# Kernel optimization log

Hardware: AMD Instinct MI355X
Metric: run time of the kernel (lower is better)

The kernel has to match this reference:

```python
import jax, jax.numpy as jnp
import numpy as np

BM = 64; BN = 64          # block_m, block_n
NKM = BM // 4; NKN = BN // 4   # tokens sampled per block (16)
# topk_newtype bands: cumulative-pooled-attention fraction -> granularity value (0 = skip block)
RATIO_BANDS = [(1, 0.05), (2, 0.15), (4, 0.25), (8, 0.5)]


def setup_inputs() -> dict:
    key = jax.random.key(0)
    kq, kk, kv, ki, kj = jax.random.split(key, 5)
    B, H, L, D = 1, 8, 4096, 64
    q = jax.random.normal(kq, (B, H, L, D), jnp.float32)
    k = jax.random.normal(kk, (B, H, L, D), jnp.float32)
    v = jax.random.normal(kv, (B, H, L, D), jnp.float32)
    # distinct in-block sample positions, shared across blocks per (B,H)
    # (mirrors torch.topk(torch.rand(B,H,1,block), sample_num))
    sample_idx_q = jnp.argsort(jax.random.uniform(ki, (B, H, BM)), axis=-1)[..., :NKM].astype(jnp.int32)
    sample_idx_k = jnp.argsort(jax.random.uniform(kj, (B, H, BN)), axis=-1)[..., :NKN].astype(jnp.int32)
    return {"q": q, "k": k, "v": v, "sample_idx_q": sample_idx_q, "sample_idx_k": sample_idx_k}


def _sample_blocks(x, idx, bs, nk):
    # x: [B,H,L,D]; idx: [B,H,nk] in-block positions -> [B,H,nb*nk,D]
    B, H, L, D = x.shape
    nb = L // bs
    xb = x.reshape(B, H, nb, bs, D)
    gidx = jnp.broadcast_to(idx[:, :, None, :, None], (B, H, nb, nk, D))
    return jnp.take_along_axis(xb, gidx, axis=3).reshape(B, H, nb * nk, D)


def _block_mask(q, k, sample_idx_q, sample_idx_k):
    # pooled downsampled attention -> per-(q_block,k_block) keep mask (topk_newtype)
    B, H, L, D = q.shape
    qb, kb = L // BM, L // BN
    sq = _sample_blocks(q, sample_idx_q, BM, NKM)  # [B,H,qb*NKM,D]
    sk = _sample_blocks(k, sample_idx_k, BN, NKN)  # [B,H,kb*NKN,D]
    scores = jnp.einsum('bhqd,bhkd->bhqk', sq, sk) / jnp.sqrt(jnp.float32(D))
    attn = jax.nn.softmax(scores, axis=-1)
    # NKM x NKN sum-pooling == block-level pooled attention mass  [B,H,qb,kb]
    pooling = attn.reshape(B, H, qb, NKM, kb, NKN).sum(axis=(3, 5))
    # rank key-blocks per q-block row by pooled mass, band by cumulative fraction
    order = jnp.argsort(-pooling, axis=-1)
    sp = jnp.take_along_axis(pooling, order, axis=-1)
    cs = jnp.cumsum(sp, axis=-1)
    frac_before = (cs - sp) / cs[..., -1:]
    val = jnp.zeros_like(sp)
    for g, hi in RATIO_BANDS[::-1]:
        val = jnp.where(frac_before < hi, jnp.float32(g), val)
    rank = jnp.argsort(order, axis=-1)          # inverse permutation
    mask_vals = jnp.take_along_axis(val, rank, axis=-1)  # [B,H,qb,kb] in {0,1,2,4,8}
    return mask_vals > 0


def reference(q, k, v, sample_idx_q, sample_idx_k):
    B, H, L, D = q.shape
    attend = _block_mask(q, k, sample_idx_q, sample_idx_k)            # [B,H,qb,kb]
    attend_tok = jnp.repeat(jnp.repeat(attend, BM, axis=2), BN, axis=3)  # [B,H,L,L]
    scores = jnp.einsum('bhqd,bhkd->bhqk', q, k) / jnp.sqrt(jnp.float32(D))
    scores = jnp.where(attend_tok, scores, jnp.float32(-1e30))
    p = jax.nn.softmax(scores, axis=-1)
    return jnp.einsum('bhqk,bhkd->bhqd', p, v)
```

## Files before the change

kernel.cpp:

```cpp
#include <hip/hip_runtime.h>
#include <hip/hip_bf16.h>

#define H_ 8
#define L_ 4096
#define D_ 64
#define NB_ 64

typedef __attribute__((ext_vector_type(8))) short bf16x8;
typedef __attribute__((ext_vector_type(4))) float f32x4;

__device__ __forceinline__ unsigned short f2bf(float x) {
    unsigned u = __float_as_uint(x);
    u += 0x7fff + ((u >> 16) & 1);
    return (unsigned short)(u >> 16);
}
__device__ __forceinline__ float bf2f(unsigned short s) {
    return __uint_as_float(((unsigned)s) << 16);
}
__device__ __forceinline__ void gload_lds16(const unsigned short* g, unsigned short* l) {
    __builtin_amdgcn_global_load_lds(
        (const __attribute__((address_space(1))) unsigned int*)(const void*)g,
        (__attribute__((address_space(3))) unsigned int*)(void*)l,
        16, 0, 0);
}

__global__ __launch_bounds__(256) void prep_kernel(
    const float* __restrict__ q, const float* __restrict__ k, const float* __restrict__ v,
    const int* __restrict__ sidxk,
    unsigned short* __restrict__ qhi, unsigned short* __restrict__ qlo,
    unsigned short* __restrict__ khi,
    unsigned short* __restrict__ vth,
    unsigned short* __restrict__ skh, unsigned short* __restrict__ skl)
{
    const int h  = blockIdx.x >> 6;
    const int tb = blockIdx.x & 63;
    const int tid = threadIdx.x;
    __shared__ float vst[64][68];

    const size_t te = ((size_t)(h*64 + tb)) << 12;
    const float4* qg = (const float4*)(q + te);
    for (int i4 = tid; i4 < 1024; i4 += 256) {
        float4 t = qg[i4];
        ushort4 hi, lo;
        hi.x = f2bf(t.x); lo.x = f2bf(t.x - bf2f(hi.x));
        hi.y = f2bf(t.y); lo.y = f2bf(t.y - bf2f(hi.y));
        hi.z = f2bf(t.z); lo.z = f2bf(t.z - bf2f(hi.z));
        hi.w = f2bf(t.w); lo.w = f2bf(t.w - bf2f(hi.w));
        *(ushort4*)(qhi + te + i4*4) = hi;
        *(ushort4*)(qlo + te + i4*4) = lo;
    }
    const float4* kg = (const float4*)(k + te);
    for (int i4 = tid; i4 < 1024; i4 += 256) {
        float4 t = kg[i4];
        int r = i4 >> 4, c4 = i4 & 15;
        int sch = (c4 >> 1) ^ ((r >> 2) & 7);
        ushort4 hi;
        hi.x = f2bf(t.x); hi.y = f2bf(t.y); hi.z = f2bf(t.z); hi.w = f2bf(t.w);
        *(ushort4*)(khi + te + r*64 + sch*8 + (c4 & 1)*4) = hi;
    }
    {
        int t = tid >> 4, d4 = tid & 15;
        int srow = tb*64 + sidxk[h*16 + t];
        float4 x = *(const float4*)(k + ((size_t)h*L_ + srow)*D_ + d4*4);
        ushort4 hi, lo;
        hi.x = f2bf(x.x); lo.x = f2bf(x.x - bf2f(hi.x));
        hi.y = f2bf(x.y); lo.y = f2bf(x.y - bf2f(hi.y));
        hi.z = f2bf(x.z); lo.z = f2bf(x.z - bf2f(hi.z));
        hi.w = f2bf(x.w); lo.w = f2bf(x.w - bf2f(hi.w));
        int sch = (d4 >> 1) ^ (t & 7);
        size_t dst = ((size_t)h*1024 + tb*16 + t)*64 + sch*8 + (d4 & 1)*4;
        *(ushort4*)(skh + dst) = hi;
        *(ushort4*)(skl + dst) = lo;
    }
    const float4* vg = (const float4*)(v + te);
    for (int i4 = tid; i4 < 1024; i4 += 256) {
        float4 t = vg[i4];
        *(float4*)&vst[i4 >> 4][(i4 & 15)*4] = t;
    }
    __syncthreads();
    for (int u = tid; u < 512; u += 256) {
        int d = u >> 3, kc8 = u & 7;
        int sch = kc8 ^ (d & 7);
        ushort4 h0, h1;
        h0.x = f2bf(vst[kc8*8+0][d]); h0.y = f2bf(vst[kc8*8+1][d]);
        h0.z = f2bf(vst[kc8*8+2][d]); h0.w = f2bf(vst[kc8*8+3][d]);
        h1.x = f2bf(vst[kc8*8+4][d]); h1.y = f2bf(vst[kc8*8+5][d]);
        h1.z = f2bf(vst[kc8*8+6][d]); h1.w = f2bf(vst[kc8*8+7][d]);
        *(ushort4*)(vth + te + d*64 + sch*8 + 0) = h0;
        *(ushort4*)(vth + te + d*64 + sch*8 + 4) = h1;
    }
}

__global__ __launch_bounds__(256, 4) void mask_mfma(
    const unsigned short* __restrict__ qhi, const unsigned short* __restrict__ qlo,
    const unsigned short* __restrict__ skh, const unsigned short* __restrict__ skl,
    const int* __restrict__ sidxq,
    unsigned long long* __restrict__ maskbits)
{
    const int h    = blockIdx.x & 7;
    const int qb   = blockIdx.x >> 3;
    const int tid  = threadIdx.x;
    const int wave = tid >> 6;
    const int lane = tid & 63;
    const int l16  = lane & 15;
    const int quad = lane >> 4;

    __shared__ __align__(16) unsigned short ch[8192];
    __shared__ __align__(16) unsigned short cl[8192];
    __shared__ float E[16][64];
    __shared__ float Z[16];
    __shared__ float pooled[64];

    for (int e = tid; e < 16*64; e += 256) (&E[0][0])[e] = 0.f;

    const int iqr = sidxq[h*16 + l16];
    const size_t qo = (((size_t)(h*64 + qb)) << 12) + (size_t)iqr*64;
    bf16x8 qh[2], ql[2];
    qh[0] = *(const bf16x8*)(qhi + qo + quad*8);
    qh[1] = *(const bf16x8*)(qhi + qo + 32 + quad*8);
    ql[0] = *(const bf16x8*)(qlo + qo + quad*8);
    ql[1] = *(const bf16x8*)(qlo + qo + 32 + quad*8);
    __syncthreads();

    for (int cc = 0; cc < 8; ++cc) {
        const bf16x8* gh = (const bf16x8*)(skh + ((size_t)h*1024 + cc*128)*64);
        const bf16x8* gl = (const bf16x8*)(skl + ((size_t)h*1024 + cc*128)*64);
        for (int i = tid; i < 1024; i += 256) {
            ((bf16x8*)ch)[i] = gh[i];
            ((bf16x8*)cl)[i] = gl[i];
        }
        __syncthreads();

        #pragma unroll
        for (int tt = 0; tt < 2; ++tt) {
            const int kb = cc*8 + wave*2 + tt;
            const int nb = (wave*2 + tt)*16;
            f32x4 sacc = (f32x4){0.f, 0.f, 0.f, 0.f};
            #pragma unroll
            for (int kc = 0; kc < 2; ++kc) {
                const int off = (nb + l16)*64 + (((kc*4 + quad) ^ (l16 & 7))*8);
                bf16x8 kh = *(const bf16x8*)&ch[off];
                bf16x8 kl = *(const bf16x8*)&cl[off];
                sacc = __builtin_amdgcn_mfma_f32_16x16x32_bf16(qh[kc], kh, sacc, 0, 0, 0);
                sacc = __builtin_amdgcn_mfma_f32_16x16x32_bf16(qh[kc], kl, sacc, 0, 0, 0);
                sacc = __builtin_amdgcn_mfma_f32_16x16x32_bf16(ql[kc], kh, sacc, 0, 0, 0);
                sacc = __builtin_amdgcn_mfma_f32_16x16x32_bf16(ql[kc], kl, sacc, 0, 0, 0);
            }
            #pragma unroll
            for (int r = 0; r < 4; ++r) {
                float p = __expf(sacc[r] * 0.125f);
                p += __shfl_xor(p, 1);
                p += __shfl_xor(p, 2);
                p += __shfl_xor(p, 4);
                p += __shfl_xor(p, 8);
                if (l16 == 0) E[quad*4 + r][kb] = p;
            }
        }
        __syncthreads();
    }

    if (tid < 16) {
        float s = 0.f;
        #pragma unroll
        for (int kb = 0; kb < 64; ++kb) s += E[tid][kb];
        Z[tid] = s;
    }
    __syncthreads();
    if (tid < 64) {
        float s = 0.f;
        #pragma unroll
        for (int t = 0; t < 16; ++t) s += E[t][tid] / Z[t];
        pooled[tid] = s;
    }
    __syncthreads();
    if (tid < 64) {
        float pi = pooled[tid];
        float tot = 0.f, bef = 0.f;
        for (int j2 = 0; j2 < 64; ++j2) {
            float pj = pooled[j2];
            tot += pj;
            if (pj > pi || (pj == pi && j2 < tid)) bef += pj;
        }
        bool att = (bef / tot) < 0.5f;
        unsigned long long bits = __ballot(att);
        if (tid == 0) maskbits[h*64 + qb] = bits;
    }
}

__global__ __launch_bounds__(256, 2) void attn_wave(
    const unsigned short* __restrict__ qhi,
    const unsigned short* __restrict__ khi,
    const unsigned short* __restrict__ vth,
    const unsigned long long* __restrict__ maskbits,
    float* __restrict__ out)
{
    const int h    = blockIdx.x & 7;
    const int qb   = blockIdx.x >> 3;
    const int tid  = threadIdx.x;
    const int wave = tid >> 6;
    const int lane = tid & 63;
    const int l16  = lane & 15;
    const int quad = lane >> 4;

    __shared__ __align__(16) char SM[66560];
    unsigned short* Qh = (unsigned short*)SM;
    unsigned short* ps = (unsigned short*)(SM + 9216 + wave*11264);

    const size_t qbase = ((size_t)(h*64 + qb)) << 12;

    for (int c = tid; c < 512; c += 256) {
        int row = c >> 3, cc = c & 7;
        int sw = cc ^ ((row >> 2) & 7);
        uint4 th = *(const uint4*)(qhi + qbase + row*64 + cc*8);
        *(uint4*)&Qh[row*72 + sw*8] = th;
    }

    unsigned long long rem = maskbits[(h << 6) + qb];
    for (int s = 0; s < wave; ++s) rem &= rem - 1;
    int cur = rem ? (int)__builtin_ctzll(rem) : -1;

    const bf16x8 ones = {0x3F80, 0x3F80, 0x3F80, 0x3F80, 0x3F80, 0x3F80, 0x3F80, 0x3F80};

    f32x4 lacc[4];
    f32x4 oacc[4][4];
    #pragma unroll
    for (int qt = 0; qt < 4; ++qt) {
        lacc[qt] = (f32x4){0.f, 0.f, 0.f, 0.f};
        #pragma unroll
        for (int dt = 0; dt < 4; ++dt) oacc[qt][dt] = (f32x4){0.f, 0.f, 0.f, 0.f};
    }

    bf16x8 kf[4][2], vf[4][2];
    if (cur >= 0) {
        const size_t tb = ((size_t)(h*64 + cur)) << 12;
        #pragma unroll
        for (int t = 0; t < 4; ++t)
            #pragma unroll
            for (int kc = 0; kc < 2; ++kc) {
                kf[t][kc] = *(const bf16x8*)(khi + tb + (l16*4 + t)*64 + (((kc*4 + quad) ^ (l16 & 7))*8));
                vf[t][kc] = *(const bf16x8*)(vth + tb + (t*16 + l16)*64 + (((kc*4 + quad) ^ (l16 & 7))*8));
            }
    }
    __syncthreads();

    while (cur >= 0) {
        rem &= rem - 1; rem &= rem - 1; rem &= rem - 1; rem &= rem - 1;
        const int nxt = rem ? (int)__builtin_ctzll(rem) : -1;

        #pragma unroll
        for (int qt = 0; qt < 4; ++qt) {
            const int xb = (qt*4 + (l16 >> 2)) & 7;
            bf16x8 ah[2];
            #pragma unroll
            for (int kc = 0; kc < 2; ++kc) {
                const int off = (qt*16 + l16)*72 + (((kc*4 + quad) ^ xb)*8);
                ah[kc] = *(const bf16x8*)&Qh[off];
            }
            f32x4 sacc[4];
            #pragma unroll
            for (int t = 0; t < 4; ++t) sacc[t] = (f32x4){0.f, 0.f, 0.f, 0.f};
            #pragma unroll
            for (int t = 0; t < 4; ++t)
                #pragma unroll
                for (int kc = 0; kc < 2; ++kc)
                    sacc[t] = __builtin_amdgcn_mfma_f32_16x16x32_bf16(ah[kc], kf[t][kc], sacc[t], 0, 0, 0);
            #pragma unroll
            for (int r = 0; r < 4; ++r) {
                float p0 = __builtin_amdgcn_exp2f(fmaf(sacc[0][r], 0.18033688f, -23.083121f));
                float p1 = __builtin_amdgcn_exp2f(fmaf(sacc[1][r], 0.18033688f, -23.083121f));
                float p2 = __builtin_amdgcn_exp2f(fmaf(sacc[2][r], 0.18033688f, -23.083121f));
                float p3 = __builtin_amdgcn_exp2f(fmaf(sacc[3][r], 0.18033688f, -23.083121f));
                __hip_bfloat162 a01 = __float22bfloat162_rn(make_float2(p0, p1));
                __hip_bfloat162 a23 = __float22bfloat162_rn(make_float2(p2, p3));
                uint2 w; w.x = *(unsigned*)&a01; w.y = *(unsigned*)&a23;
                *(uint2*)&ps[(qt*16 + quad*4 + r)*88 + l16*4] = w;
            }
        }
        if (nxt >= 0) {
            const size_t tb = ((size_t)(h*64 + nxt)) << 12;
            #pragma unroll
            for (int t = 0; t < 4; ++t)
                #pragma unroll
                for (int kc = 0; kc < 2; ++kc)
                    kf[t][kc] = *(const bf16x8*)(khi + tb + (l16*4 + t)*64 + (((kc*4 + quad) ^ (l16 & 7))*8));
        }
        #pragma unroll
        for (int qt = 0; qt < 4; ++qt) {
            bf16x8 pf0 = *(const bf16x8*)&ps[(qt*16 + l16)*88 + quad*8];
            bf16x8 pf1 = *(const bf16x8*)&ps[(qt*16 + l16)*88 + 32 + quad*8];
            lacc[qt] = __builtin_amdgcn_mfma_f32_16x16x32_bf16(pf0, ones, lacc[qt], 0, 0, 0);
            lacc[qt] = __builtin_amdgcn_mfma_f32_16x16x32_bf16(pf1, ones, lacc[qt], 0, 0, 0);
            #pragma unroll
            for (int dt = 0; dt < 4; ++dt) {
                oacc[qt][dt] = __builtin_amdgcn_mfma_f32_16x16x32_bf16(pf0, vf[dt][0], oacc[qt][dt], 0, 0, 0);
                oacc[qt][dt] = __builtin_amdgcn_mfma_f32_16x16x32_bf16(pf1, vf[dt][1], oacc[qt][dt], 0, 0, 0);
            }
        }
        if (nxt >= 0) {
            const size_t tb = ((size_t)(h*64 + nxt)) << 12;
            #pragma unroll
            for (int dt = 0; dt < 4; ++dt)
                #pragma unroll
                for (int kc = 0; kc < 2; ++kc)
                    vf[dt][kc] = *(const bf16x8*)(vth + tb + (dt*16 + l16)*64 + (((kc*4 + quad) ^ (l16 & 7))*8));
        }
        cur = nxt;
    }

    __syncthreads();
    float* ored = (float*)SM;
    float* lred = (float*)(SM + 65536);
    #pragma unroll
    for (int qt = 0; qt < 4; ++qt) {
        #pragma unroll
        for (int dt = 0; dt < 4; ++dt)
            #pragma unroll
            for (int r = 0; r < 4; ++r)
                ored[wave*4096 + (qt*16 + quad*4 + r)*64 + dt*16 + l16] = oacc[qt][dt][r];
        if (l16 == 0) {
            #pragma unroll
            for (int r = 0; r < 4; ++r)
                lred[wave*64 + qt*16 + quad*4 + r] = lacc[qt][r];
        }
    }
    __syncthreads();
    {
        const int row = tid >> 2;
        const int d0  = (tid & 3) << 4;
        float l = lred[row] + lred[64 + row] + lred[128 + row] + lred[192 + row];
        float inv = 1.f / l;
        float* og = out + ((size_t)h*L_ + (size_t)qb*64 + row)*D_ + d0;
        #pragma unroll
        for (int j = 0; j < 16; j += 4) {
            float4 a = *(float4*)&ored[0*4096 + row*64 + d0 + j];
            float4 b = *(float4*)&ored[1*4096 + row*64 + d0 + j];
            float4 c = *(float4*)&ored[2*4096 + row*64 + d0 + j];
            float4 d = *(float4*)&ored[3*4096 + row*64 + d0 + j];
            float4 rr;
            rr.x = (a.x + b.x + c.x + d.x) * inv;
            rr.y = (a.y + b.y + c.y + d.y) * inv;
            rr.z = (a.z + b.z + c.z + d.z) * inv;
            rr.w = (a.w + b.w + c.w + d.w) * inv;
            *(float4*)(og + j) = rr;
        }
    }
}

__global__ __launch_bounds__(256, 4) void mask_kernel4(
    const float* __restrict__ q, const float* __restrict__ k,
    const int* __restrict__ sidxq, const int* __restrict__ sidxk,
    unsigned long long* __restrict__ maskbits)
{
    const int h   = blockIdx.x >> 6;
    const int qb  = blockIdx.x & 63;
    const int tid = threadIdx.x;
    const int rg  = tid >> 5;
    const int cg  = tid & 31;

    __shared__ float sq[16][68];
    __shared__ float skc[128][68];
    __shared__ float E[16][64];
    __shared__ float Z[16];
    __shared__ float pooled[64];
    __shared__ int iq[16], ik[16];

    if (tid < 16) { iq[tid] = sidxq[h*16 + tid]; ik[tid] = sidxk[h*16 + tid]; }
    for (int e = tid; e < 16*64; e += 256) (&E[0][0])[e] = 0.f;
    __syncthreads();
    {
        int j = tid >> 4, d4 = tid & 15;
        int grow = h*L_ + qb*64 + iq[j];
        *(float4*)&sq[j][d4*4] = *(const float4*)(q + (size_t)grow*D_ + d4*4);
    }
    for (int cc = 0; cc < 8; ++cc) {
        for (int i = tid; i < 2048; i += 256) {
            int col = i >> 4, d4 = i & 15;
            int colg = cc*128 + col;
            int grow = h*L_ + (colg >> 4)*64 + ik[colg & 15];
            *(float4*)&skc[col][d4*4] = *(const float4*)(k + (size_t)grow*D_ + d4*4);
        }
        __syncthreads();
        float acc[2][4] = {{0.f,0.f,0.f,0.f},{0.f,0.f,0.f,0.f}};
        #pragma unroll 4
        for (int d4 = 0; d4 < 16; ++d4) {
            float4 qv0 = *(const float4*)&sq[rg*2 + 0][d4*4];
            float4 qv1 = *(const float4*)&sq[rg*2 + 1][d4*4];
            #pragma unroll
            for (int j = 0; j < 4; ++j) {
                float4 kv = *(const float4*)&skc[cg + 32*j][d4*4];
                acc[0][j] += qv0.x*kv.x + qv0.y*kv.y + qv0.z*kv.z + qv0.w*kv.w;
                acc[1][j] += qv1.x*kv.x + qv1.y*kv.y + qv1.z*kv.z + qv1.w*kv.w;
            }
        }
        #pragma unroll
        for (int j = 0; j < 4; ++j) {
            int kb = cc*8 + (cg >> 4) + 2*j;
            #pragma unroll
            for (int i = 0; i < 2; ++i) {
                float p = __expf(acc[i][j] * 0.125f);
                p += __shfl_xor(p, 1);
                p += __shfl_xor(p, 2);
                p += __shfl_xor(p, 4);
                p += __shfl_xor(p, 8);
                if ((cg & 15) == 0) E[rg*2 + i][kb] += p;
            }
        }
        __syncthreads();
    }
    if (tid < 16) {
        float s = 0.f;
        #pragma unroll
        for (int kb = 0; kb < 64; ++kb) s += E[tid][kb];
        Z[tid] = s;
    }
    __syncthreads();
    if (tid < 64) {
        float s = 0.f;
        #pragma unroll
        for (int t = 0; t < 16; ++t) s += E[t][tid] / Z[t];
        pooled[tid] = s;
    }
    __syncthreads();
    if (tid < 64) {
        float pi = pooled[tid];
        float tot = 0.f, bef = 0.f;
        for (int j2 = 0; j2 < 64; ++j2) {
            float pj = pooled[j2];
            tot += pj;
            if (pj > pi || (pj == pi && j2 < tid)) bef += pj;
        }
        bool att = (bef / tot) < 0.5f;
        unsigned long long bits = __ballot(att);
        if (tid == 0) maskbits[h*64 + qb] = bits;
    }
}

__global__ __launch_bounds__(256, 3) void attn_v3(
    const float* __restrict__ q, const float* __restrict__ k, const float* __restrict__ v,
    const unsigned long long* __restrict__ maskbits, float* __restrict__ out)
{
    const int h = blockIdx.x >> 6, qb = blockIdx.x & 63;
    const int tid = threadIdx.x, wave = tid >> 6, lane = tid & 63;
    const int l16 = lane & 15, quad = lane >> 4;
    __shared__ __align__(16) unsigned short ks_hi[64][72];
    __shared__ __align__(16) unsigned short ks_lo[64][72];
    __shared__ __align__(16) unsigned short vt_hi[64][72];
    __shared__ __align__(16) unsigned short vt_lo[64][72];
    __shared__ __align__(16) unsigned short ps[4][16][72];

    const float4* qg = (const float4*)(q + ((size_t)h*L_ + (size_t)qb*64)*D_);
    for (int i4 = tid; i4 < 1024; i4 += 256) {
        float4 t = qg[i4];
        int r = i4 >> 4, c = (i4 & 15) << 2;
        ushort4 hi, lo;
        hi.x = f2bf(t.x); lo.x = f2bf(t.x - bf2f(hi.x));
        hi.y = f2bf(t.y); lo.y = f2bf(t.y - bf2f(hi.y));
        hi.z = f2bf(t.z); lo.z = f2bf(t.z - bf2f(hi.z));
        hi.w = f2bf(t.w); lo.w = f2bf(t.w - bf2f(hi.w));
        *(ushort4*)&ks_hi[r][c] = hi;
        *(ushort4*)&ks_lo[r][c] = lo;
    }
    const unsigned long long bm = maskbits[(h << 6) + qb];
    __syncthreads();
    bf16x8 qhi2[2], qlo2[2];
    #pragma unroll
    for (int kc = 0; kc < 2; ++kc) {
        qhi2[kc] = *(const bf16x8*)&ks_hi[wave*16 + l16][kc*32 + quad*8];
        qlo2[kc] = *(const bf16x8*)&ks_lo[wave*16 + l16][kc*32 + quad*8];
    }
    __syncthreads();
    float m_i[4], l_i[4];
    f32x4 oacc[4];
    #pragma unroll
    for (int r = 0; r < 4; ++r) { m_i[r] = -1e30f; l_i[r] = 0.f; }
    #pragma unroll
    for (int t = 0; t < 4; ++t) oacc[t] = (f32x4){0.f, 0.f, 0.f, 0.f};
    for (int kb = 0; kb < 64; ++kb) {
        if (!((bm >> kb) & 1ull)) continue;
        const float4* kg = (const float4*)(k + ((size_t)h*L_ + (size_t)kb*64)*D_);
        const float*  vg = v + ((size_t)h*L_ + (size_t)kb*64)*D_;
        for (int i4 = tid; i4 < 1024; i4 += 256) {
            float4 t = kg[i4];
            int r = i4 >> 4, c = (i4 & 15) << 2;
            ushort4 hi, lo;
            hi.x = f2bf(t.x); lo.x = f2bf(t.x - bf2f(hi.x));
            hi.y = f2bf(t.y); lo.y = f2bf(t.y - bf2f(hi.y));
            hi.z = f2bf(t.z); lo.z = f2bf(t.z - bf2f(hi.z));
            hi.w = f2bf(t.w); lo.w = f2bf(t.w - bf2f(hi.w));
            *(ushort4*)&ks_hi[r][c] = hi;
            *(ushort4*)&ks_lo[r][c] = lo;
        }
        for (int tsk = tid; tsk < 512; tsk += 256) {
            int rp = tsk >> 4;
            int c  = (tsk & 15) << 2;
            float4 a0 = *(const float4*)(vg + (size_t)(2*rp)*D_ + c);
            float4 a1 = *(const float4*)(vg + (size_t)(2*rp+1)*D_ + c);
            #pragma unroll
            for (int j = 0; j < 4; ++j) {
                float x0 = (j==0)?a0.x:(j==1)?a0.y:(j==2)?a0.z:a0.w;
                float x1 = (j==0)?a1.x:(j==1)?a1.y:(j==2)?a1.z:a1.w;
                unsigned short h0 = f2bf(x0), h1b = f2bf(x1);
                *(unsigned*)&vt_hi[c+j][2*rp] = (unsigned)h0 | ((unsigned)h1b << 16);
                unsigned short lo0 = f2bf(x0 - bf2f(h0)), lo1 = f2bf(x1 - bf2f(h1b));
                *(unsigned*)&vt_lo[c+j][2*rp] = (unsigned)lo0 | ((unsigned)lo1 << 16);
            }
        }
        __syncthreads();
        f32x4 sacc[4];
        #pragma unroll
        for (int t = 0; t < 4; ++t) sacc[t] = (f32x4){0.f, 0.f, 0.f, 0.f};
        #pragma unroll
        for (int t = 0; t < 4; ++t) {
            #pragma unroll
            for (int kc = 0; kc < 2; ++kc) {
                bf16x8 khi2 = *(const bf16x8*)&ks_hi[t*16 + l16][kc*32 + quad*8];
                bf16x8 klo2 = *(const bf16x8*)&ks_lo[t*16 + l16][kc*32 + quad*8];
                sacc[t] = __builtin_amdgcn_mfma_f32_16x16x32_bf16(qhi2[kc], khi2, sacc[t], 0, 0, 0);
                sacc[t] = __builtin_amdgcn_mfma_f32_16x16x32_bf16(qhi2[kc], klo2, sacc[t], 0, 0, 0);
                sacc[t] = __builtin_amdgcn_mfma_f32_16x16x32_bf16(qlo2[kc], khi2, sacc[t], 0, 0, 0);
            }
        }
        #pragma unroll
        for (int t = 0; t < 4; ++t) sacc[t] *= 0.125f;
        float rowmax[4];
        #pragma unroll
        for (int r = 0; r < 4; ++r)
            rowmax[r] = fmaxf(fmaxf(sacc[0][r], sacc[1][r]), fmaxf(sacc[2][r], sacc[3][r]));
        #pragma unroll
        for (int off = 1; off < 16; off <<= 1)
            #pragma unroll
            for (int r = 0; r < 4; ++r)
                rowmax[r] = fmaxf(rowmax[r], __shfl_xor(rowmax[r], off));
        float al[4], rs[4];
        #pragma unroll
        for (int r = 0; r < 4; ++r) {
            float mnew = fmaxf(m_i[r], rowmax[r]);
            al[r] = __expf(m_i[r] - mnew);
            m_i[r] = mnew;
            float acc = 0.f;
            #pragma unroll
            for (int t = 0; t < 4; ++t) {
                float p = __expf(sacc[t][r] - mnew);
                unsigned short pb = f2bf(p);
                ps[wave][quad*4 + r][t*16 + l16] = pb;
                acc += bf2f(pb);
            }
            rs[r] = acc;
        }
        #pragma unroll
        for (int off = 1; off < 16; off <<= 1)
            #pragma unroll
            for (int r = 0; r < 4; ++r)
                rs[r] += __shfl_xor(rs[r], off);
        #pragma unroll
        for (int r = 0; r < 4; ++r) l_i[r] = l_i[r] * al[r] + rs[r];
        #pragma unroll
        for (int t = 0; t < 4; ++t)
            #pragma unroll
            for (int r = 0; r < 4; ++r) oacc[t][r] *= al[r];
        bf16x8 pf[2];
        #pragma unroll
        for (int kc = 0; kc < 2; ++kc)
            pf[kc] = *(const bf16x8*)&ps[wave][l16][kc*32 + quad*8];
        #pragma unroll
        for (int t = 0; t < 4; ++t) {
            #pragma unroll
            for (int kc = 0; kc < 2; ++kc) {
                bf16x8 vhif = *(const bf16x8*)&vt_hi[t*16 + l16][kc*32 + quad*8];
                bf16x8 vlof = *(const bf16x8*)&vt_lo[t*16 + l16][kc*32 + quad*8];
                oacc[t] = __builtin_amdgcn_mfma_f32_16x16x32_bf16(pf[kc], vhif, oacc[t], 0, 0, 0);
                oacc[t] = __builtin_amdgcn_mfma_f32_16x16x32_bf16(pf[kc], vlof, oacc[t], 0, 0, 0);
            }
        }
        __syncthreads();
    }
    float* og = out + ((size_t)h*L_ + (size_t)qb*64)*D_ + (size_t)(wave*16 + quad*4)*D_;
    #pragma unroll
    for (int r = 0; r < 4; ++r) {
        float inv = 1.f / l_i[r];
        #pragma unroll
        for (int t = 0; t < 4; ++t)
            og[(size_t)r*D_ + t*16 + l16] = oacc[t][r] * inv;
    }
}

extern "C" void kernel_launch(void* const* d_in, const int* in_sizes, int n_in,
                              void* d_out, int out_size, void* d_ws, size_t ws_size,
                              hipStream_t stream) {
    const float* q = (const float*)d_in[0];
    const float* k = (const float*)d_in[1];
    const float* v = (const float*)d_in[2];
    const int* siq = (const int*)d_in[3];
    const int* sik = (const int*)d_in[4];
    float* out = (float*)d_out;

    char* ws = (char*)d_ws;
    unsigned long long* mask = (unsigned long long*)ws;
    const size_t TEN = (size_t)H_*L_*D_;
    const size_t SKN = (size_t)H_*1024*64;
    unsigned short* qhi = (unsigned short*)(ws + 4096);
    unsigned short* qlo = qhi + TEN;
    unsigned short* khi = qlo + TEN;
    unsigned short* vth = khi + TEN;
    unsigned short* skh = vth + TEN;
    unsigned short* skl = skh + SKN;
    const size_t need = 4096 + (4*TEN + 2*SKN)*sizeof(unsigned short);

    if (ws_size >= need) {
        prep_kernel<<<dim3(H_*NB_), dim3(256), 0, stream>>>(q, k, v, sik, qhi, qlo, khi, vth, skh, skl);
        mask_mfma<<<dim3(H_*NB_), dim3(256), 0, stream>>>(qhi, qlo, skh, skl, siq, mask);
        attn_wave<<<dim3(H_*NB_), dim3(256), 0, stream>>>(qhi, khi, vth, mask, out);
    } else {
        mask_kernel4<<<dim3(H_*NB_), dim3(256), 0, stream>>>(q, k, siq, sik, mask);
        attn_v3<<<dim3(H_*NB_), dim3(256), 0, stream>>>(q, k, v, mask, out);
    }
}
```

Measured before the change: 133.4 us.

## Split attention block across 8 waves by query half and key stride

The attention kernel now launches 512 threads per block. Waves are split into two query halves times four key-block strides, so each wave handles 32 query rows instead of 64. K and V fragments share one register array: V is loaded mid-iteration after the QK product for the second query tile, which lowers register pressure so the launch bound can target 4 blocks per CU. The cost is that each wave issues its own K/V global loads, doubling K/V fetch traffic per block. It also cuts the independent work available per wave to hide load latency.

Result: slower. 138.1 us (+3.5%).

```diff
diff --git a/kernel.cpp b/kernel.cpp
--- a/kernel.cpp
+++ b/kernel.cpp
@@ -16,12 +16,6 @@
 }
 __device__ __forceinline__ float bf2f(unsigned short s) {
     return __uint_as_float(((unsigned)s) << 16);
-}
-__device__ __forceinline__ void gload_lds16(const unsigned short* g, unsigned short* l) {
-    __builtin_amdgcn_global_load_lds(
-        (const __attribute__((address_space(1))) unsigned int*)(const void*)g,
-        (__attribute__((address_space(3))) unsigned int*)(void*)l,
-        16, 0, 0);
 }
 
 __global__ __launch_bounds__(256) void prep_kernel(
@@ -187,7 +181,7 @@
     }
 }
 
-__global__ __launch_bounds__(256, 2) void attn_wave(
+__global__ __launch_bounds__(512, 4) void attn_qsplit(
     const unsigned short* __restrict__ qhi,
     const unsigned short* __restrict__ khi,
     const unsigned short* __restrict__ vth,
@@ -201,108 +195,118 @@
     const int lane = tid & 63;
     const int l16  = lane & 15;
     const int quad = lane >> 4;
+    const int qhalf = wave >> 2;
+    const int kw    = wave & 3;
 
     __shared__ __align__(16) char SM[66560];
     unsigned short* Qh = (unsigned short*)SM;
-    unsigned short* ps = (unsigned short*)(SM + 9216 + wave*11264);
+    unsigned short* ps = (unsigned short*)(SM + 9216 + wave*5632);
 
     const size_t qbase = ((size_t)(h*64 + qb)) << 12;
 
-    for (int c = tid; c < 512; c += 256) {
-        int row = c >> 3, cc = c & 7;
+    {
+        int row = tid >> 3, cc = tid & 7;
         int sw = cc ^ ((row >> 2) & 7);
-        uint4 th = *(const uint4*)(qhi + qbase + row*64 + cc*8);
-        *(uint4*)&Qh[row*72 + sw*8] = th;
+        *(uint4*)&Qh[row*72 + sw*8] = *(const uint4*)(qhi + qbase + row*64 + cc*8);
     }
 
     unsigned long long rem = maskbits[(h << 6) + qb];
-    for (int s = 0; s < wave; ++s) rem &= rem - 1;
+    for (int s = 0; s < kw; ++s) rem &= rem - 1;
     int cur = rem ? (int)__builtin_ctzll(rem) : -1;
 
     const bf16x8 ones = {0x3F80, 0x3F80, 0x3F80, 0x3F80, 0x3F80, 0x3F80, 0x3F80, 0x3F80};
 
-    f32x4 lacc[4];
-    f32x4 oacc[4][4];
+    f32x4 lacc[2];
+    f32x4 oacc[2][4];
     #pragma unroll
-    for (int qt = 0; qt < 4; ++qt) {
+    for (int qt = 0; qt < 2; ++qt) {
         lacc[qt] = (f32x4){0.f, 0.f, 0.f, 0.f};
         #pragma unroll
         for (int dt = 0; dt < 4; ++dt) oacc[qt][dt] = (f32x4){0.f, 0.f, 0.f, 0.f};
     }
 
-    bf16x8 kf[4][2], vf[4][2];
+    const unsigned swz  = (unsigned)((quad ^ (l16 & 7)) * 16);
+    const unsigned koff = (unsigned)l16*512 + swz;
+    const unsigned voff = (unsigned)l16*128 + swz;
+
+    bf16x8 kv[4][2];
     if (cur >= 0) {
-        const size_t tb = ((size_t)(h*64 + cur)) << 12;
-        #pragma unroll
-        for (int t = 0; t < 4; ++t)
-            #pragma unroll
-            for (int kc = 0; kc < 2; ++kc) {
-                kf[t][kc] = *(const bf16x8*)(khi + tb + (l16*4 + t)*64 + (((kc*4 + quad) ^ (l16 & 7))*8));
-                vf[t][kc] = *(const bf16x8*)(vth + tb + (t*16 + l16)*64 + (((kc*4 + quad) ^ (l16 & 7))*8));
-            }
-    }
-    __syncthreads();
+        const char* kb = (const char*)khi + (((size_t)(h*64 + cur)) << 13);
+        #pragma unroll
+        for (int t = 0; t < 4; ++t) {
+            kv[t][0] = *(const bf16x8*)(kb + (koff + t*128));
+            kv[t][1] = *(const bf16x8*)(kb + ((koff ^ 64) + t*128));
+        }
+    }
+    __syncthreads();
+
+    auto qk = [&](int gqt, f32x4* sacc) {
+        const int xb = (gqt*4 + (l16 >> 2)) & 7;
+        bf16x8 ah[2];
+        #pragma unroll
+        for (int kc = 0; kc < 2; ++kc)
+            ah[kc] = *(const bf16x8*)&Qh[(gqt*16 + l16)*72 + (((kc*4 + quad) ^ xb)*8)];
+        #pragma unroll
+        for (int t = 0; t < 4; ++t) {
+            f32x4 s = (f32x4){0.f, 0.f, 0.f, 0.f};
+            s = __builtin_amdgcn_mfma_f32_16x16x32_bf16(ah[0], kv[t][0], s, 0, 0, 0);
+            s = __builtin_amdgcn_mfma_f32_16x16x32_bf16(ah[1], kv[t][1], s, 0, 0, 0);
+            sacc[t] = s;
+        }
+    };
+    auto sm = [&](int qt, f32x4* sacc) {
+        #pragma unroll
+        for (int r = 0; r < 4; ++r) {
+            float p0 = __builtin_amdgcn_exp2f(fmaf(sacc[0][r], 0.18033688f, -23.083121f));
+            float p1 = __builtin_amdgcn_exp2f(fmaf(sacc[1][r], 0.18033688f, -23.083121f));
+            float p2 = __builtin_amdgcn_exp2f(fmaf(sacc[2][r], 0.18033688f, -23.083121f));
+            float p3 = __builtin_amdgcn_exp2f(fmaf(sacc[3][r], 0.18033688f, -23.083121f));
+            __hip_bfloat162 a01 = __float22bfloat162_rn(make_float2(p0, p1));
+            __hip_bfloat162 a23 = __float22bfloat162_rn(make_float2(p2, p3));
+            uint2 w; w.x = *(unsigned*)&a01; w.y = *(unsigned*)&a23;
+            *(uint2*)&ps[(qt*16 + quad*4 + r)*88 + l16*4] = w;
+        }
+    };
 
     while (cur >= 0) {
         rem &= rem - 1; rem &= rem - 1; rem &= rem - 1; rem &= rem - 1;
         const int nxt = rem ? (int)__builtin_ctzll(rem) : -1;
-
-        #pragma unroll
-        for (int qt = 0; qt < 4; ++qt) {
-            const int xb = (qt*4 + (l16 >> 2)) & 7;
-            bf16x8 ah[2];
-            #pragma unroll
-            for (int kc = 0; kc < 2; ++kc) {
-                const int off = (qt*16 + l16)*72 + (((kc*4 + quad) ^ xb)*8);
-                ah[kc] = *(const bf16x8*)&Qh[off];
-            }
-            f32x4 sacc[4];
-            #pragma unroll
-            for (int t = 0; t < 4; ++t) sacc[t] = (f32x4){0.f, 0.f, 0.f, 0.f};
-            #pragma unroll
-            for (int t = 0; t < 4; ++t)
-                #pragma unroll
-                for (int kc = 0; kc < 2; ++kc)
-                    sacc[t] = __builtin_amdgcn_mfma_f32_16x16x32_bf16(ah[kc], kf[t][kc], sacc[t], 0, 0, 0);
-            #pragma unroll
-            for (int r = 0; r < 4; ++r) {
-                float p0 = __builtin_amdgcn_exp2f(fmaf(sacc[0][r], 0.18033688f, -23.083121f));
-                float p1 = __builtin_amdgcn_exp2f(fmaf(sacc[1][r], 0.18033688f, -23.083121f));
-                float p2 = __builtin_amdgcn_exp2f(fmaf(sacc[2][r], 0.18033688f, -23.083121f));
-                float p3 = __builtin_amdgcn_exp2f(fmaf(sacc[3][r], 0.18033688f, -23.083121f));
-                __hip_bfloat162 a01 = __float22bfloat162_rn(make_float2(p0, p1));
-                __hip_bfloat162 a23 = __float22bfloat162_rn(make_float2(p2, p3));
-                uint2 w; w.x = *(unsigned*)&a01; w.y = *(unsigned*)&a23;
-                *(uint2*)&ps[(qt*16 + quad*4 + r)*88 + l16*4] = w;
-            }
-        }
-        if (nxt >= 0) {
-            const size_t tb = ((size_t)(h*64 + nxt)) << 12;
-            #pragma unroll
-            for (int t = 0; t < 4; ++t)
-                #pragma unroll
-                for (int kc = 0; kc < 2; ++kc)
-                    kf[t][kc] = *(const bf16x8*)(khi + tb + (l16*4 + t)*64 + (((kc*4 + quad) ^ (l16 & 7))*8));
-        }
-        #pragma unroll
-        for (int qt = 0; qt < 4; ++qt) {
+        const char* vb = (const char*)vth + (((size_t)(h*64 + cur)) << 13);
+
+        {
+            f32x4 s0[4];
+            qk(qhalf*2 + 0, s0);
+            sm(0, s0);
+        }
+        {
+            f32x4 s1[4];
+            qk(qhalf*2 + 1, s1);
+            #pragma unroll
+            for (int dt = 0; dt < 4; ++dt) {
+                kv[dt][0] = *(const bf16x8*)(vb + (voff + dt*2048));
+                kv[dt][1] = *(const bf16x8*)(vb + ((voff ^ 64) + dt*2048));
+            }
+            sm(1, s1);
+        }
+        #pragma unroll
+        for (int qt = 0; qt < 2; ++qt) {
             bf16x8 pf0 = *(const bf16x8*)&ps[(qt*16 + l16)*88 + quad*8];
             bf16x8 pf1 = *(const bf16x8*)&ps[(qt*16 + l16)*88 + 32 + quad*8];
             lacc[qt] = __builtin_amdgcn_mfma_f32_16x16x32_bf16(pf0, ones, lacc[qt], 0, 0, 0);
             lacc[qt] = __builtin_amdgcn_mfma_f32_16x16x32_bf16(pf1, ones, lacc[qt], 0, 0, 0);
             #pragma unroll
             for (int dt = 0; dt < 4; ++dt) {
-                oacc[qt][dt] = __builtin_amdgcn_mfma_f32_16x16x32_bf16(pf0, vf[dt][0], oacc[qt][dt], 0, 0, 0);
-                oacc[qt][dt] = __builtin_amdgcn_mfma_f32_16x16x32_bf16(pf1, vf[dt][1], oacc[qt][dt], 0, 0, 0);
+                oacc[qt][dt] = __builtin_amdgcn_mfma_f32_16x16x32_bf16(pf0, kv[dt][0], oacc[qt][dt], 0, 0, 0);
+                oacc[qt][dt] = __builtin_amdgcn_mfma_f32_16x16x32_bf16(pf1, kv[dt][1], oacc[qt][dt], 0, 0, 0);
             }
         }
         if (nxt >= 0) {
-            const size_t tb = ((size_t)(h*64 + nxt)) << 12;
-            #pragma unroll
-            for (int dt = 0; dt < 4; ++dt)
-                #pragma unroll
-                for (int kc = 0; kc < 2; ++kc)
-                    vf[dt][kc] = *(const bf16x8*)(vth + tb + (dt*16 + l16)*64 + (((kc*4 + quad) ^ (l16 & 7))*8));
+            const char* kb = (const char*)khi + (((size_t)(h*64 + nxt)) << 13);
+            #pragma unroll
+            for (int t = 0; t < 4; ++t) {
+                kv[t][0] = *(const bf16x8*)(kb + (koff + t*128));
+                kv[t][1] = *(const bf16x8*)(kb + ((koff ^ 64) + t*128));
+            }
         }
         cur = nxt;
     }
@@ -311,27 +315,28 @@
     float* ored = (float*)SM;
     float* lred = (float*)(SM + 65536);
     #pragma unroll
-    for (int qt = 0; qt < 4; ++qt) {
+    for (int qt = 0; qt < 2; ++qt) {
+        const int gr0 = qhalf*32 + qt*16 + quad*4;
         #pragma unroll
         for (int dt = 0; dt < 4; ++dt)
             #pragma unroll
             for (int r = 0; r < 4; ++r)
-                ored[wave*4096 + (qt*16 + quad*4 + r)*64 + dt*16 + l16] = oacc[qt][dt][r];
+                ored[(kw*64 + gr0 + r)*64 + dt*16 + l16] = oacc[qt][dt][r];
         if (l16 == 0) {
             #pragma unroll
             for (int r = 0; r < 4; ++r)
-                lred[wave*64 + qt*16 + quad*4 + r] = lacc[qt][r];
+                lred[kw*64 + gr0 + r] = lacc[qt][r];
         }
     }
     __syncthreads();
     {
-        const int row = tid >> 2;
-        const int d0  = (tid & 3) << 4;
+        const int row = tid >> 3;
+        const int d0  = (tid & 7) << 3;
         float l = lred[row] + lred[64 + row] + lred[128 + row] + lred[192 + row];
         float inv = 1.f / l;
         float* og = out + ((size_t)h*L_ + (size_t)qb*64 + row)*D_ + d0;
         #pragma unroll
-        for (int j = 0; j < 16; j += 4) {
+        for (int j = 0; j < 8; j += 4) {
             float4 a = *(float4*)&ored[0*4096 + row*64 + d0 + j];
             float4 b = *(float4*)&ored[1*4096 + row*64 + d0 + j];
             float4 c = *(float4*)&ored[2*4096 + row*64 + d0 + j];
@@ -609,7 +614,7 @@
     if (ws_size >= need) {
         prep_kernel<<<dim3(H_*NB_), dim3(256), 0, stream>>>(q, k, v, sik, qhi, qlo, khi, vth, skh, skl);
         mask_mfma<<<dim3(H_*NB_), dim3(256), 0, stream>>>(qhi, qlo, skh, skl, siq, mask);
-        attn_wave<<<dim3(H_*NB_), dim3(256), 0, stream>>>(qhi, khi, vth, mask, out);
+        attn_qsplit<<<dim3(H_*NB_), dim3(512), 0, stream>>>(qhi, khi, vth, mask, out);
     } else {
         mask_kernel4<<<dim3(H_*NB_), dim3(256), 0, stream>>>(q, k, siq, sik, mask);
         attn_v3<<<dim3(H_*NB_), dim3(256), 0, stream>>>(q, k, v, mask, out);
```

## Split attention work across waves by query half and key-block parity

Applied to the files above, without the earlier changes.

Before, each of the four waves took every fourth active key block and handled all 64 query rows. Now waves are arranged 2x2: each wave handles 32 query rows and alternate key blocks. This halves per-wave accumulators and per-wave P scratch, cuts shared memory to about 33KB and raises launch bounds to 3 blocks per CU, and only two partial results are reduced at the end. The cost is that each K/V block fragment is loaded from global by two waves, doubling K/V register-load traffic per block.

Result: slower. 137.2 us (+2.8%).

```diff
diff --git a/kernel.cpp b/kernel.cpp
--- a/kernel.cpp
+++ b/kernel.cpp
@@ -16,12 +16,6 @@
 }
 __device__ __forceinline__ float bf2f(unsigned short s) {
     return __uint_as_float(((unsigned)s) << 16);
-}
-__device__ __forceinline__ void gload_lds16(const unsigned short* g, unsigned short* l) {
-    __builtin_amdgcn_global_load_lds(
-        (const __attribute__((address_space(1))) unsigned int*)(const void*)g,
-        (__attribute__((address_space(3))) unsigned int*)(void*)l,
-        16, 0, 0);
 }
 
 __global__ __launch_bounds__(256) void prep_kernel(
@@ -187,7 +181,7 @@
     }
 }
 
-__global__ __launch_bounds__(256, 2) void attn_wave(
+__global__ __launch_bounds__(256, 3) void attn_qh(
     const unsigned short* __restrict__ qhi,
     const unsigned short* __restrict__ khi,
     const unsigned short* __restrict__ vth,
@@ -201,30 +195,31 @@
     const int lane = tid & 63;
     const int l16  = lane & 15;
     const int quad = lane >> 4;
-
-    __shared__ __align__(16) char SM[66560];
+    const int qhalf = wave >> 1;
+    const int kw    = wave & 1;
+
+    __shared__ __align__(16) char SM[33280];
     unsigned short* Qh = (unsigned short*)SM;
-    unsigned short* ps = (unsigned short*)(SM + 9216 + wave*11264);
+    unsigned short* ps = (unsigned short*)(SM + 9216 + wave*5632);
 
     const size_t qbase = ((size_t)(h*64 + qb)) << 12;
 
     for (int c = tid; c < 512; c += 256) {
         int row = c >> 3, cc = c & 7;
         int sw = cc ^ ((row >> 2) & 7);
-        uint4 th = *(const uint4*)(qhi + qbase + row*64 + cc*8);
-        *(uint4*)&Qh[row*72 + sw*8] = th;
+        *(uint4*)&Qh[row*72 + sw*8] = *(const uint4*)(qhi + qbase + row*64 + cc*8);
     }
 
     unsigned long long rem = maskbits[(h << 6) + qb];
-    for (int s = 0; s < wave; ++s) rem &= rem - 1;
+    if (kw && rem) rem &= rem - 1;
     int cur = rem ? (int)__builtin_ctzll(rem) : -1;
 
     const bf16x8 ones = {0x3F80, 0x3F80, 0x3F80, 0x3F80, 0x3F80, 0x3F80, 0x3F80, 0x3F80};
 
-    f32x4 lacc[4];
-    f32x4 oacc[4][4];
+    f32x4 lacc[2];
+    f32x4 oacc[2][4];
     #pragma unroll
-    for (int qt = 0; qt < 4; ++qt) {
+    for (int qt = 0; qt < 2; ++qt) {
         lacc[qt] = (f32x4){0.f, 0.f, 0.f, 0.f};
         #pragma unroll
         for (int dt = 0; dt < 4; ++dt) oacc[qt][dt] = (f32x4){0.f, 0.f, 0.f, 0.f};
@@ -244,26 +239,25 @@
     __syncthreads();
 
     while (cur >= 0) {
-        rem &= rem - 1; rem &= rem - 1; rem &= rem - 1; rem &= rem - 1;
+        rem &= rem - 1; rem &= rem - 1;
         const int nxt = rem ? (int)__builtin_ctzll(rem) : -1;
 
         #pragma unroll
-        for (int qt = 0; qt < 4; ++qt) {
-            const int xb = (qt*4 + (l16 >> 2)) & 7;
+        for (int lqt = 0; lqt < 2; ++lqt) {
+            const int gqt = qhalf*2 + lqt;
+            const int xb = (gqt*4 + (l16 >> 2)) & 7;
             bf16x8 ah[2];
             #pragma unroll
-            for (int kc = 0; kc < 2; ++kc) {
-                const int off = (qt*16 + l16)*72 + (((kc*4 + quad) ^ xb)*8);
-                ah[kc] = *(const bf16x8*)&Qh[off];
-            }
+            for (int kc = 0; kc < 2; ++kc)
+                ah[kc] = *(const bf16x8*)&Qh[(gqt*16 + l16)*72 + (((kc*4 + quad) ^ xb)*8)];
             f32x4 sacc[4];
             #pragma unroll
-            for (int t = 0; t < 4; ++t) sacc[t] = (f32x4){0.f, 0.f, 0.f, 0.f};
-            #pragma unroll
-            for (int t = 0; t < 4; ++t)
-                #pragma unroll
-                for (int kc = 0; kc < 2; ++kc)
-                    sacc[t] = __builtin_amdgcn_mfma_f32_16x16x32_bf16(ah[kc], kf[t][kc], sacc[t], 0, 0, 0);
+            for (int t = 0; t < 4; ++t) {
+                f32x4 s = (f32x4){0.f, 0.f, 0.f, 0.f};
+                s = __builtin_amdgcn_mfma_f32_16x16x32_bf16(ah[0], kf[t][0], s, 0, 0, 0);
+                s = __builtin_amdgcn_mfma_f32_16x16x32_bf16(ah[1], kf[t][1], s, 0, 0, 0);
+                sacc[t] = s;
+            }
             #pragma unroll
             for (int r = 0; r < 4; ++r) {
                 float p0 = __builtin_amdgcn_exp2f(fmaf(sacc[0][r], 0.18033688f, -23.083121f));
@@ -273,7 +267,7 @@
                 __hip_bfloat162 a01 = __float22bfloat162_rn(make_float2(p0, p1));
                 __hip_bfloat162 a23 = __float22bfloat162_rn(make_float2(p2, p3));
                 uint2 w; w.x = *(unsigned*)&a01; w.y = *(unsigned*)&a23;
-                *(uint2*)&ps[(qt*16 + quad*4 + r)*88 + l16*4] = w;
+                *(uint2*)&ps[(lqt*16 + quad*4 + r)*88 + l16*4] = w;
             }
         }
         if (nxt >= 0) {
@@ -285,15 +279,15 @@
                     kf[t][kc] = *(const bf16x8*)(khi + tb + (l16*4 + t)*64 + (((kc*4 + quad) ^ (l16 & 7))*8));
         }
         #pragma unroll
-        for (int qt = 0; qt < 4; ++qt) {
-            bf16x8 pf0 = *(const bf16x8*)&ps[(qt*16 + l16)*88 + quad*8];
-            bf16x8 pf1 = *(const bf16x8*)&ps[(qt*16 + l16)*88 + 32 + quad*8];
-            lacc[qt] = __builtin_amdgcn_mfma_f32_16x16x32_bf16(pf0, ones, lacc[qt], 0, 0, 0);
-            lacc[qt] = __builtin_amdgcn_mfma_f32_16x16x32_bf16(pf1, ones, lacc[qt], 0, 0, 0);
+        for (int lqt = 0; lqt < 2; ++lqt) {
+            bf16x8 pf0 = *(const bf16x8*)&ps[(lqt*16 + l16)*88 + quad*8];
+            bf16x8 pf1 = *(const bf16x8*)&ps[(lqt*16 + l16)*88 + 32 + quad*8];
+            lacc[lqt] = __builtin_amdgcn_mfma_f32_16x16x32_bf16(pf0, ones, lacc[lqt], 0, 0, 0);
+            lacc[lqt] = __builtin_amdgcn_mfma_f32_16x16x32_bf16(pf1, ones, lacc[lqt], 0, 0, 0);
             #pragma unroll
             for (int dt = 0; dt < 4; ++dt) {
-                oacc[qt][dt] = __builtin_amdgcn_mfma_f32_16x16x32_bf16(pf0, vf[dt][0], oacc[qt][dt], 0, 0, 0);
-                oacc[qt][dt] = __builtin_amdgcn_mfma_f32_16x16x32_bf16(pf1, vf[dt][1], oacc[qt][dt], 0, 0, 0);
+                oacc[lqt][dt] = __builtin_amdgcn_mfma_f32_16x16x32_bf16(pf0, vf[dt][0], oacc[lqt][dt], 0, 0, 0);
+                oacc[lqt][dt] = __builtin_amdgcn_mfma_f32_16x16x32_bf16(pf1, vf[dt][1], oacc[lqt][dt], 0, 0, 0);
             }
         }
         if (nxt >= 0) {
@@ -309,38 +303,37 @@
 
     __syncthreads();
     float* ored = (float*)SM;
-    float* lred = (float*)(SM + 65536);
+    float* lred = (float*)(SM + 32768);
     #pragma unroll
-    for (int qt = 0; qt < 4; ++qt) {
+    for (int lqt = 0; lqt < 2; ++lqt) {
+        const int gr0 = qhalf*32 + lqt*16 + quad*4;
         #pragma unroll
         for (int dt = 0; dt < 4; ++dt)
             #pragma unroll
             for (int r = 0; r < 4; ++r)
-                ored[wave*4096 + (qt*16 + quad*4 + r)*64 + dt*16 + l16] = oacc[qt][dt][r];
+                ored[(kw*64 + gr0 + r)*64 + dt*16 + l16] = oacc[lqt][dt][r];
         if (l16 == 0) {
             #pragma unroll
             for (int r = 0; r < 4; ++r)
-                lred[wave*64 + qt*16 + quad*4 + r] = lacc[qt][r];
+                lred[kw*64 + gr0 + r] = lacc[lqt][r];
         }
     }
     __syncthreads();
     {
         const int row = tid >> 2;
         const int d0  = (tid & 3) << 4;
-        float l = lred[row] + lred[64 + row] + lred[128 + row] + lred[192 + row];
+        float l = lred[row] + lred[64 + row];
         float inv = 1.f / l;
         float* og = out + ((size_t)h*L_ + (size_t)qb*64 + row)*D_ + d0;
         #pragma unroll
         for (int j = 0; j < 16; j += 4) {
-            float4 a = *(float4*)&ored[0*4096 + row*64 + d0 + j];
-            float4 b = *(float4*)&ored[1*4096 + row*64 + d0 + j];
-            float4 c = *(float4*)&ored[2*4096 + row*64 + d0 + j];
-            float4 d = *(float4*)&ored[3*4096 + row*64 + d0 + j];
+            float4 a = *(float4*)&ored[row*64 + d0 + j];
+            float4 b = *(float4*)&ored[4096 + row*64 + d0 + j];
             float4 rr;
-            rr.x = (a.x + b.x + c.x + d.x) * inv;
-            rr.y = (a.y + b.y + c.y + d.y) * inv;
-            rr.z = (a.z + b.z + c.z + d.z) * inv;
-            rr.w = (a.w + b.w + c.w + d.w) * inv;
+            rr.x = (a.x + b.x) * inv;
+            rr.y = (a.y + b.y) * inv;
+            rr.z = (a.z + b.z) * inv;
+            rr.w = (a.w + b.w) * inv;
             *(float4*)(og + j) = rr;
         }
     }
@@ -609,7 +602,7 @@
     if (ws_size >= need) {
         prep_kernel<<<dim3(H_*NB_), dim3(256), 0, stream>>>(q, k, v, sik, qhi, qlo, khi, vth, skh, skl);
         mask_mfma<<<dim3(H_*NB_), dim3(256), 0, stream>>>(qhi, qlo, skh, skl, siq, mask);
-        attn_wave<<<dim3(H_*NB_), dim3(256), 0, stream>>>(qhi, khi, vth, mask, out);
+        attn_qh<<<dim3(H_*NB_), dim3(256), 0, stream>>>(qhi, khi, vth, mask, out);
     } else {
         mask_kernel4<<<dim3(H_*NB_), dim3(256), 0, stream>>>(q, k, siq, sik, mask);
         attn_v3<<<dim3(H_*NB_), dim3(256), 0, stream>>>(q, k, v, mask, out);
```
